# Optimization experiments

Measured on AMD Instinct MI355X. Metric: run time of the kernel, lower is better.

The kernel has to match this reference:

```python
import jax, jax.numpy as jnp
import numpy as np

B, S, DIM, H = 8, 1024, 768, 12
HD = DIM // H  # head_dim = 64
SCALE = HD ** -0.5


def setup_inputs() -> dict:
    key = jax.random.key(0)
    ks = jax.random.split(key, 9)
    std = DIM ** -0.5
    x = jax.random.normal(ks[0], (B, S, DIM), dtype=jnp.float32)
    Wq = jax.random.normal(ks[1], (DIM, DIM), dtype=jnp.float32) * std
    bq = jax.random.normal(ks[2], (DIM,), dtype=jnp.float32) * 0.01
    Wk = jax.random.normal(ks[3], (DIM, DIM), dtype=jnp.float32) * std
    bk = jax.random.normal(ks[4], (DIM,), dtype=jnp.float32) * 0.01
    Wv = jax.random.normal(ks[5], (DIM, DIM), dtype=jnp.float32) * std
    bv = jax.random.normal(ks[6], (DIM,), dtype=jnp.float32) * 0.01
    Wp = jax.random.normal(ks[7], (DIM, DIM), dtype=jnp.float32) * std
    bp = jax.random.normal(ks[8], (DIM,), dtype=jnp.float32) * 0.01
    return {"x": x, "Wq": Wq, "bq": bq, "Wk": Wk, "bk": bk,
            "Wv": Wv, "bv": bv, "Wp": Wp, "bp": bp}


def _split_heads(t):
    # [b, s, (n d)] -> [b, n, s, d]
    b, s, _ = t.shape
    return t.reshape(b, s, H, HD).transpose(0, 2, 1, 3)


def reference(x, Wq, bq, Wk, bk, Wv, bv, Wp, bp):
    q = _split_heads(x @ Wq + bq)
    k = _split_heads(x @ Wk + bk)
    v = _split_heads(x @ Wv + bv)
    attn = jnp.einsum('bnqd,bnkd->bnqk', q, k) * SCALE
    attn = jax.nn.softmax(attn, axis=-1)
    o = jnp.einsum('bnqk,bnkd->bnqd', attn, v)
    o = o.transpose(0, 2, 1, 3).reshape(x.shape[0], x.shape[1], DIM)
    return o @ Wp + bp
```

## Files before the change

kernel.cpp:

```cpp
#include <hip/hip_runtime.h>
#include <hip/hip_bf16.h>
#include <cstdint>

#define B_    8
#define S_    1024
#define DIM_  768
#define H_    12
#define HD_   64
#define QL2S_ 0.1803368801111204f

typedef __attribute__((ext_vector_type(8))) __bf16 bf16x8;
typedef __attribute__((ext_vector_type(4))) __bf16 bf16x4;
typedef __attribute__((ext_vector_type(4))) short i16x4;
typedef __attribute__((ext_vector_type(4))) float  f32x4;

__device__ __forceinline__ short f2bf(float f) {
  union { float f; uint32_t u; } a;
  a.f = f;
  uint32_t u = a.u;
  uint32_t r = (u + 0x7FFFu + ((u >> 16) & 1u)) >> 16;
  return (short)r;
}

__device__ __forceinline__ float exp2a(float x) {
  float r;
  asm("v_exp_f32 %0, %1\n\ts_nop 1" : "=v"(r) : "v"(x));
  return r;
}

__device__ __forceinline__ f32x4 mfma16(bf16x4 a, bf16x4 b, f32x4 c) {
#if __has_builtin(__builtin_amdgcn_mfma_f32_16x16x16_bf16)
  return __builtin_amdgcn_mfma_f32_16x16x16_bf16(a, b, c, 0, 0, 0);
#else
  union { bf16x4 h; i16x4 s; } ua, ub;
  ua.h = a; ub.h = b;
  return __builtin_amdgcn_mfma_f32_16x16x16bf16_1k(ua.s, ub.s, c, 0, 0, 0);
#endif
}

__device__ __forceinline__ void gll16(const void* g, void* l) {
  __builtin_amdgcn_global_load_lds((const __attribute__((address_space(1))) void*)g,
                                   (__attribute__((address_space(3))) void*)l, 16, 0, 0);
}

__device__ __forceinline__ int swz(int row, int col) {
  return row * 128 + ((((col >> 3) ^ (row & 7)) & 7) << 4) + ((col & 7) << 1);
}

__global__ __launch_bounds__(256) void k_prep(const float* __restrict__ x,
                                              const float* __restrict__ W0,
                                              const float* __restrict__ W1,
                                              const float* __restrict__ W2,
                                              const float* __restrict__ W3,
                                              short* __restrict__ xb,
                                              short* o0, short* o1,
                                              short* o2, short* o3) {
  const int tx = threadIdx.x, ty = threadIdx.y;
  if (blockIdx.z == 4) {
    const int tid = ty * 32 + tx;
    int i = (blockIdx.y * 24 + blockIdx.x) * 256 + tid;
    const int n4 = 8192 * 768 / 4;
    const int nthr = 24 * 24 * 256;
    for (; i < n4; i += nthr) {
      const float4 v = ((const float4*)x)[i];
      short4 o;
      o.x = f2bf(v.x); o.y = f2bf(v.y); o.z = f2bf(v.z); o.w = f2bf(v.w);
      ((short4*)xb)[i] = o;
    }
    return;
  }
  const float* in = blockIdx.z == 0 ? W0 : blockIdx.z == 1 ? W1 : blockIdx.z == 2 ? W2 : W3;
  short* out = blockIdx.z == 0 ? o0 : blockIdx.z == 1 ? o1 : blockIdx.z == 2 ? o2 : o3;
  __shared__ float tile[32][33];
  const int bx = blockIdx.x * 32, by = blockIdx.y * 32;
#pragma unroll
  for (int j = 0; j < 32; j += 8)
    tile[ty + j][tx] = in[(size_t)(by + ty + j) * DIM_ + bx + tx];
  __syncthreads();
#pragma unroll
  for (int j = 0; j < 32; j += 8)
    out[(size_t)(bx + ty + j) * DIM_ + by + tx] = f2bf(tile[tx][ty + j]);
}

template <int MODE, bool QS>
__device__ __forceinline__ void gemm_body(char* smem,
                                          const short* __restrict__ A,
                                          const short* __restrict__ Bt,
                                          const float* __restrict__ bias,
                                          void* __restrict__ out,
                                          int bm, int bn) {
  char* As = smem;
  char* Bs = smem + 32768;
  const int tid = threadIdx.x;
  const int l = tid & 63, w = tid >> 6;
  const int hi = l >> 4, lo = l & 15;
  const int wr = w >> 1, wc = w & 1;

  auto stageA = [&](int ks, int bo) {
#pragma unroll
    for (int i = 0; i < 4; ++i) {
      const int gl = i * 256 + tid;
      const int row = gl >> 3;
      const int g = (gl & 7) ^ (row & 7);
      gll16(A + (size_t)(bm * 128 + row) * DIM_ + ks * 64 + g * 8, As + bo + gl * 16);
    }
  };
  auto stageB = [&](int ks, int bo) {
#pragma unroll
    for (int i = 0; i < 4; ++i) {
      const int gl = i * 256 + tid;
      const int row = gl >> 3;
      const int g = (gl & 7) ^ (row & 7);
      gll16(Bt + (size_t)(bn * 128 + row) * DIM_ + ks * 64 + g * 8, Bs + bo + gl * 16);
    }
  };

  f32x4 acc[4][4];
  const f32x4 zz = {0.f, 0.f, 0.f, 0.f};
#pragma unroll
  for (int m = 0; m < 4; ++m)
#pragma unroll
    for (int n = 0; n < 4; ++n) acc[m][n] = zz;

  stageA(0, 0);
  stageB(0, 0);
  __syncthreads();

  for (int ks = 0; ks < 12; ++ks) {
    const int cu = (ks & 1) << 14;
    if (ks < 11) { stageA(ks + 1, cu ^ 16384); stageB(ks + 1, cu ^ 16384); }
#pragma unroll
    for (int kk = 0; kk < 2; ++kk) {
      bf16x8 a[4], b[4];
#pragma unroll
      for (int m = 0; m < 4; ++m)
        a[m] = *(const bf16x8*)(As + cu + swz(wr * 64 + m * 16 + lo, kk * 32 + hi * 8));
#pragma unroll
      for (int n = 0; n < 4; ++n)
        b[n] = *(const bf16x8*)(Bs + cu + swz(wc * 64 + n * 16 + lo, kk * 32 + hi * 8));
#pragma unroll
      for (int m = 0; m < 4; ++m)
#pragma unroll
        for (int n = 0; n < 4; ++n)
          acc[m][n] = __builtin_amdgcn_mfma_f32_16x16x32_bf16(a[m], b[n], acc[m][n], 0, 0, 0);
    }
    __syncthreads();
  }

#pragma unroll
  for (int m = 0; m < 4; ++m) {
#pragma unroll
    for (int n = 0; n < 4; ++n) {
#pragma unroll
      for (int r = 0; r < 4; ++r) {
        const int R = bm * 128 + wr * 64 + m * 16 + hi * 4 + r;
        const int C = bn * 128 + wc * 64 + n * 16 + lo;
        float v = acc[m][n][r] + bias[MODE == 1 ? R : C];
        if (QS) v *= QL2S_;
        if (MODE == 0) {
          ((short*)out)[((size_t)((R >> 10) * H_ + (C >> 6)) * S_ + (R & 1023)) * HD_ + (C & 63)] = f2bf(v);
        } else if (MODE == 1) {
          ((short*)out)[((size_t)((C >> 10) * H_ + (R >> 6)) * HD_ + (R & 63)) * S_ + (C & 1023)] = f2bf(v);
        } else {
          ((float*)out)[(size_t)R * DIM_ + C] = v;
        }
      }
    }
  }
}

__global__ __launch_bounds__(256, 2) void k_gemm_qkv(const short* __restrict__ xb,
                                                     const short* __restrict__ WqT,
                                                     const short* __restrict__ WkT,
                                                     const short* __restrict__ WvT,
                                                     const float* __restrict__ bq,
                                                     const float* __restrict__ bk,
                                                     const float* __restrict__ bv,
                                                     short* qo, short* ko, short* vo) {
  __shared__ alignas(16) char smem[65536];
  if (blockIdx.z == 0)
    gemm_body<0, true>(smem, xb, WqT, bq, qo, blockIdx.x, blockIdx.y);
  else if (blockIdx.z == 1)
    gemm_body<0, false>(smem, xb, WkT, bk, ko, blockIdx.x, blockIdx.y);
  else
    gemm_body<1, false>(smem, WvT, xb, bv, vo, blockIdx.y, blockIdx.x);
}

__global__ __launch_bounds__(256, 2) void k_gemm_proj(const short* __restrict__ A,
                                                      const short* __restrict__ Bt,
                                                      const float* __restrict__ bias,
                                                      float* out) {
  __shared__ alignas(16) char smem[65536];
  gemm_body<2, false>(smem, A, Bt, bias, out, blockIdx.y, blockIdx.x);
}

__global__ __launch_bounds__(256, 4) void k_attn(const short* __restrict__ qw,
                                                 const short* __restrict__ kw,
                                                 const short* __restrict__ vtw,
                                                 short* __restrict__ ow) {
  __shared__ alignas(16) char smem[32768];
  char* Kb = smem;
  char* Vb = smem + 16384;
  const int tid = threadIdx.x;
  const int l = tid & 63, w = tid >> 6;
  const int hi = l >> 4, lo = l & 15;
  const int qt = blockIdx.x / 96;
  const int bh = blockIdx.x % 96;

  const short* qg = qw  + (size_t)bh * (S_ * HD_) + (qt * 128) * HD_;
  const short* kg = kw  + (size_t)bh * (S_ * HD_);
  const short* vg = vtw + (size_t)bh * (S_ * HD_);

  auto stage = [&](int T, int bufo) {
#pragma unroll
    for (int i = 0; i < 2; ++i) {
      const int gl = i * 256 + tid;
      const int row = gl >> 3;
      const int g = (gl & 7) ^ (row & 7);
      gll16(kg + (T * 64 + row) * 64 + g * 8, Kb + bufo + gl * 16);
    }
#pragma unroll
    for (int i = 0; i < 2; ++i) {
      const int gl = i * 256 + tid;
      const int row = gl >> 3;
      const int g = (gl & 7) ^ (row & 7);
      gll16(vg + row * 1024 + T * 64 + g * 8, Vb + bufo + gl * 16);
    }
  };

  bf16x8 aQ[2][2];
#pragma unroll
  for (int m = 0; m < 2; ++m)
#pragma unroll
    for (int kk = 0; kk < 2; ++kk)
      aQ[m][kk] = *(const bf16x8*)(qg + (w * 32 + m * 16 + lo) * HD_ + kk * 32 + hi * 8);

  f32x4 o_acc[2][4];
  const f32x4 zz = {0.f, 0.f, 0.f, 0.f};
#pragma unroll
  for (int m = 0; m < 2; ++m)
#pragma unroll
    for (int db = 0; db < 4; ++db) o_acc[m][db] = zz;
  float lsum[2] = {0.f, 0.f};

  stage(0, 0);
  __syncthreads();

  for (int t = 0; t < 16; ++t) {
    const int cu = (t & 1) << 13;
    if (t < 15) stage(t + 1, cu ^ 8192);

    f32x4 sacc[2][4];
#pragma unroll
    for (int m = 0; m < 2; ++m)
#pragma unroll
      for (int nb = 0; nb < 4; ++nb) sacc[m][nb] = zz;
    __builtin_amdgcn_s_setprio(1);
#pragma unroll
    for (int kk = 0; kk < 2; ++kk) {
#pragma unroll
      for (int nb = 0; nb < 4; ++nb) {
        const bf16x8 bK = *(const bf16x8*)(Kb + cu + swz(nb * 16 + lo, kk * 32 + hi * 8));
#pragma unroll
        for (int m = 0; m < 2; ++m)
          sacc[m][nb] = __builtin_amdgcn_mfma_f32_16x16x32_bf16(bK, aQ[m][kk], sacc[m][nb], 0, 0, 0);
      }
    }
    __builtin_amdgcn_s_setprio(0);

#pragma unroll
    for (int nb = 0; nb < 4; ++nb) {
      bf16x4 pa[2];
#pragma unroll
      for (int m = 0; m < 2; ++m) {
        const float p0 = exp2a(sacc[m][nb][0] - 1.0f);
        const float p1 = exp2a(sacc[m][nb][1] - 1.0f);
        const float p2 = exp2a(sacc[m][nb][2] - 1.0f);
        const float p3 = exp2a(sacc[m][nb][3] - 1.0f);
        lsum[m] += (p0 + p1) + (p2 + p3);
        pa[m][0] = (__bf16)p0;
        pa[m][1] = (__bf16)p1;
        pa[m][2] = (__bf16)p2;
        pa[m][3] = (__bf16)p3;
      }
#pragma unroll
      for (int db = 0; db < 4; ++db) {
        const bf16x4 bV = *(const bf16x4*)(Vb + cu + swz(db * 16 + lo, nb * 16 + hi * 4));
#pragma unroll
        for (int m = 0; m < 2; ++m)
          o_acc[m][db] = mfma16(pa[m], bV, o_acc[m][db]);
      }
    }

    __syncthreads();
  }

  float lF[2];
#pragma unroll
  for (int m = 0; m < 2; ++m) {
    float s = lsum[m];
    s += __shfl_xor(s, 16, 64);
    s += __shfl_xor(s, 32, 64);
    lF[m] = s;
  }
  const int b = bh / H_, h = bh % H_;
#pragma unroll
  for (int m = 0; m < 2; ++m) {
#pragma unroll
    for (int r = 0; r < 4; ++r) {
      const float lr = __shfl(lF[m], hi * 4 + r, 64);
      const float inv = 1.0f / lr;
      const int sg = qt * 128 + w * 32 + m * 16 + hi * 4 + r;
#pragma unroll
      for (int db = 0; db < 4; ++db)
        ow[((size_t)(b * S_ + sg)) * DIM_ + h * HD_ + db * 16 + lo] = f2bf(o_acc[m][db][r] * inv);
    }
  }
}

extern "C" void kernel_launch(void* const* d_in, const int* in_sizes, int n_in,
                              void* d_out, int out_size, void* d_ws, size_t ws_size,
                              hipStream_t stream) {
  const float* x  = (const float*)d_in[0];
  const float* Wq = (const float*)d_in[1];
  const float* bq = (const float*)d_in[2];
  const float* Wk = (const float*)d_in[3];
  const float* bk = (const float*)d_in[4];
  const float* Wv = (const float*)d_in[5];
  const float* bv = (const float*)d_in[6];
  const float* Wp = (const float*)d_in[7];
  const float* bp = (const float*)d_in[8];

  char* ws = (char*)d_ws;
  size_t off = 0;
  auto alloc = [&](size_t bytes) {
    char* p = ws + off;
    off += (bytes + 255) & ~(size_t)255;
    return p;
  };
  short* xb  = (short*)alloc((size_t)8192 * 768 * 2);
  short* WqT = (short*)alloc((size_t)768 * 768 * 2);
  short* WkT = (short*)alloc((size_t)768 * 768 * 2);
  short* WvT = (short*)alloc((size_t)768 * 768 * 2);
  short* WpT = (short*)alloc((size_t)768 * 768 * 2);
  short* qwv = (short*)alloc((size_t)96 * 1024 * 64 * 2);
  short* kwv = (short*)alloc((size_t)96 * 1024 * 64 * 2);
  short* vtw = (short*)alloc((size_t)96 * 1024 * 64 * 2);
  short* owv = (short*)alloc((size_t)8192 * 768 * 2);

  dim3 tb(32, 8), tg(24, 24, 5);
  k_prep<<<tg, tb, 0, stream>>>(x, Wq, Wk, Wv, Wp, xb, WqT, WkT, WvT, WpT);

  k_gemm_qkv<<<dim3(64, 6, 3), 256, 0, stream>>>(xb, WqT, WkT, WvT, bq, bk, bv, qwv, kwv, vtw);

  k_attn<<<B_ * H_ * (S_ / 128), 256, 0, stream>>>(qwv, kwv, vtw, owv);

  k_gemm_proj<<<dim3(6, 64), 256, 0, stream>>>(owv, WpT, bp, (float*)d_out);
}
```

Baseline: 101.9 us.

## Prefetch two stages ahead with explicit vmcnt waits in GEMM and attention loops

Both the projection GEMM and the attention kernel now issue loads for two tiles before the loop and refill a buffer right after it is consumed. Each iteration waits with a partial s_waitcnt vmcnt and raw s_barrier instead of a full __syncthreads drain. The aim is to keep a full tile of global-to-LDS loads in flight during compute, hiding memory latency. The code depends on exact per-thread load counts (8 and 4) matching the vmcnt arguments, and the sched_barriers limit compiler reordering.

Measured after the change: 106.0 us. +4.1%, slower.

```diff
diff --git a/kernel.cpp b/kernel.cpp
--- a/kernel.cpp
+++ b/kernel.cpp
@@ -8,6 +8,12 @@
 #define H_    12
 #define HD_   64
 #define QL2S_ 0.1803368801111204f
+
+#define VMCNT(n) do { asm volatile("s_waitcnt vmcnt(" #n ")" ::: "memory"); \
+                      __builtin_amdgcn_sched_barrier(0); } while (0)
+#define BAR() do { __builtin_amdgcn_sched_barrier(0); \
+                   __builtin_amdgcn_s_barrier(); \
+                   __builtin_amdgcn_sched_barrier(0); } while (0)
 
 typedef __attribute__((ext_vector_type(8))) __bf16 bf16x8;
 typedef __attribute__((ext_vector_type(4))) __bf16 bf16x4;
@@ -96,7 +102,7 @@
   const int hi = l >> 4, lo = l & 15;
   const int wr = w >> 1, wc = w & 1;
 
-  auto stageA = [&](int ks, int bo) {
+  auto stage = [&](int ks, int bo) {
 #pragma unroll
     for (int i = 0; i < 4; ++i) {
       const int gl = i * 256 + tid;
@@ -104,8 +110,6 @@
       const int g = (gl & 7) ^ (row & 7);
       gll16(A + (size_t)(bm * 128 + row) * DIM_ + ks * 64 + g * 8, As + bo + gl * 16);
     }
-  };
-  auto stageB = [&](int ks, int bo) {
 #pragma unroll
     for (int i = 0; i < 4; ++i) {
       const int gl = i * 256 + tid;
@@ -122,13 +126,7 @@
 #pragma unroll
     for (int n = 0; n < 4; ++n) acc[m][n] = zz;
 
-  stageA(0, 0);
-  stageB(0, 0);
-  __syncthreads();
-
-  for (int ks = 0; ks < 12; ++ks) {
-    const int cu = (ks & 1) << 14;
-    if (ks < 11) { stageA(ks + 1, cu ^ 16384); stageB(ks + 1, cu ^ 16384); }
+  auto compute = [&](int cu) {
 #pragma unroll
     for (int kk = 0; kk < 2; ++kk) {
       bf16x8 a[4], b[4];
@@ -144,8 +142,21 @@
         for (int n = 0; n < 4; ++n)
           acc[m][n] = __builtin_amdgcn_mfma_f32_16x16x32_bf16(a[m], b[n], acc[m][n], 0, 0, 0);
     }
-    __syncthreads();
-  }
+  };
+
+  stage(0, 0);
+  stage(1, 16384);
+  for (int ks = 0; ks < 11; ++ks) {
+    const int cu = (ks & 1) << 14;
+    VMCNT(8);
+    BAR();
+    compute(cu);
+    BAR();
+    if (ks < 10) stage(ks + 2, cu);
+  }
+  VMCNT(0);
+  BAR();
+  compute(1 << 14);
 
 #pragma unroll
   for (int m = 0; m < 4; ++m) {
@@ -243,13 +254,7 @@
     for (int db = 0; db < 4; ++db) o_acc[m][db] = zz;
   float lsum[2] = {0.f, 0.f};
 
-  stage(0, 0);
-  __syncthreads();
-
-  for (int t = 0; t < 16; ++t) {
-    const int cu = (t & 1) << 13;
-    if (t < 15) stage(t + 1, cu ^ 8192);
-
+  auto tile = [&](int cu) {
     f32x4 sacc[2][4];
 #pragma unroll
     for (int m = 0; m < 2; ++m)
@@ -291,9 +296,21 @@
           o_acc[m][db] = mfma16(pa[m], bV, o_acc[m][db]);
       }
     }
-
-    __syncthreads();
-  }
+  };
+
+  stage(0, 0);
+  stage(1, 8192);
+  for (int t = 0; t < 15; ++t) {
+    const int cu = (t & 1) << 13;
+    VMCNT(4);
+    BAR();
+    tile(cu);
+    BAR();
+    if (t < 14) stage(t + 2, cu);
+  }
+  VMCNT(0);
+  BAR();
+  tile(8192);
 
   float lF[2];
 #pragma unroll
```
